# Optimization experiments

Measured on AMD Instinct MI355X. Metric: run time of the kernel, lower is better.

## Reference

```python
import jax, jax.numpy as jnp
import numpy as np

B, T, D, H, E = 2, 1024, 1024, 4096, 8


def setup_inputs() -> dict:
    key = jax.random.key(0)
    ks = jax.random.split(key, 6)
    x = jax.random.normal(ks[0], (B, T, D), dtype=jnp.float32)
    padding_mask = jnp.zeros((B, T), dtype=bool)
    # Gate: Linear(D, E, bias=False) -> weight (E, D)
    Wg = jax.random.normal(ks[1], (E, D), dtype=jnp.float32) * (1.0 / np.sqrt(D))
    # Stacked expert FFN params (torch Linear layout: weight (out, in))
    W1 = jax.random.normal(ks[2], (E, H, D), dtype=jnp.float32) * (1.0 / np.sqrt(D))
    b1 = jax.random.normal(ks[3], (E, H), dtype=jnp.float32) * 0.01
    W2 = jax.random.normal(ks[4], (E, D, H), dtype=jnp.float32) * (1.0 / np.sqrt(H))
    b2 = jax.random.normal(ks[5], (E, D), dtype=jnp.float32) * 0.01
    return {"x": x, "padding_mask": padding_mask, "Wg": Wg, "W1": W1, "b1": b1, "W2": W2, "b2": b2}


def _top2_gate(xt, pm, Wg):
    # xt: (nt, D) flattened tokens, pm: (nt,) bool padding mask
    nt, ec = xt.shape[0], Wg.shape[0]
    logits = (xt @ Wg.T).astype(jnp.float32)            # use_fp32=True
    gate_value = jax.nn.softmax(logits, axis=-1)        # (nt, E)
    gate_value = jnp.where(pm[:, None], 0.0, gate_value)
    top2_idx = jax.lax.top_k(gate_value, 2)[1]          # (nt, 2)
    keep = jax.nn.one_hot(top2_idx, ec, dtype=bool).any(axis=1)  # (nt, E) True at top1/top2
    gate_weights = jnp.where(keep, gate_value, 0.0)
    s = gate_weights.sum(axis=1, keepdims=True)
    s = jnp.where(s == 0.0, 1.0, s)
    gate_weights = gate_weights / s
    # load-balance loss: fraction of top-1 assignments vs mean gate prob per expert
    nt_real = (~pm).sum().astype(jnp.float32)
    top1_counts = (jax.nn.one_hot(top2_idx[:, 0], ec, dtype=jnp.float32)
                   * (~pm)[:, None].astype(jnp.float32)).sum(axis=0)  # (E,)
    lb_loss = ec * ((top1_counts / nt_real) * (gate_value.sum(axis=0) / nt_real)).sum()
    return lb_loss, gate_weights, gate_value


def reference(x, padding_mask, Wg, W1, b1, W2, b2):
    Bx, Tx, Dx = x.shape
    xt = x.reshape(-1, Dx)                   # (nt, D)
    pm = padding_mask.reshape(-1)            # (nt,)
    lb_loss, gw, gate_value = _top2_gate(xt, pm, Wg)
    gw = gw.astype(x.dtype)                  # (nt, E)
    # Expert FFNs (dense over experts; routing weights are zero except top-2)
    h = jax.nn.relu(jnp.einsum('nd,ehd->neh', xt, W1) + b1)   # (nt, E, H)
    y = jnp.einsum('neh,edh->ned', h, W2) + b2                # (nt, E, D)
    out = jnp.einsum('ne,ned->nd', gw, y).reshape(Bx, Tx, Dx)
    return out, gate_value, lb_loss
```

## Files before the change

kernel.cpp:

```cpp
#include <hip/hip_runtime.h>
#include <hip/hip_bf16.h>
#include <stdint.h>


#define NTOK 2048
#define DDIM 1024
#define HDIM 4096
#define NEXP 8
#define KSPLIT 2

typedef float  f32x4  __attribute__((ext_vector_type(4)));
typedef __bf16 bf16x8 __attribute__((ext_vector_type(8)));
typedef __bf16 bf16x4 __attribute__((ext_vector_type(4)));

typedef const __attribute__((address_space(1))) void g1_t;
typedef __attribute__((address_space(3))) void l3_t;
__device__ __forceinline__ void gld16(const void* g, void* l) {
  __builtin_amdgcn_global_load_lds((g1_t*)g, (l3_t*)l, 16, 0, 0);
}

__global__ void init_kernel(int* fill) {
  int t = threadIdx.x;
  if (t < NEXP) fill[t] = 0;
}

__global__ __launch_bounds__(256)
void zero_y_kernel(float* __restrict__ y) {
  size_t i = (size_t)blockIdx.x * 256 + threadIdx.x;
  ((f32x4*)y)[i] = (f32x4){0.f, 0.f, 0.f, 0.f};
}

__global__ __launch_bounds__(256)
void gate_kernel(const float* __restrict__ x, const unsigned char* __restrict__ pmask,
                 const float* __restrict__ Wg, float* __restrict__ gate_out,
                 int* __restrict__ tix, float* __restrict__ twt,
                 __bf16* __restrict__ xbf)
{
  int wave = threadIdx.x >> 6, lane = threadIdx.x & 63;
  int t = blockIdx.x * 4 + wave;
  const f32x4* x4 = (const f32x4*)(x + (size_t)t * DDIM);
  const f32x4* w4 = (const f32x4*)Wg;
  bf16x4* xb4 = (bf16x4*)(xbf + (size_t)t * DDIM);
  float acc[NEXP];
#pragma unroll
  for (int e = 0; e < NEXP; ++e) acc[e] = 0.f;
#pragma unroll
  for (int i = 0; i < 4; ++i) {
    f32x4 xv = x4[i * 64 + lane];
    bf16x4 xo;
#pragma unroll
    for (int q = 0; q < 4; ++q) xo[q] = (__bf16)xv[q];
    xb4[i * 64 + lane] = xo;
#pragma unroll
    for (int e = 0; e < NEXP; ++e) {
      f32x4 wv = w4[e * 256 + i * 64 + lane];
      acc[e] += xv[0]*wv[0] + xv[1]*wv[1] + xv[2]*wv[2] + xv[3]*wv[3];
    }
  }
#pragma unroll
  for (int e = 0; e < NEXP; ++e) {
    float v = acc[e];
#pragma unroll
    for (int off = 32; off > 0; off >>= 1) v += __shfl_xor(v, off, 64);
    acc[e] = v;
  }
  if (lane == 0) {
    bool pm = pmask[t] != 0;
    float m = acc[0];
#pragma unroll
    for (int e = 1; e < NEXP; ++e) m = fmaxf(m, acc[e]);
    float g[NEXP]; float s = 0.f;
#pragma unroll
    for (int e = 0; e < NEXP; ++e) { g[e] = expf(acc[e] - m); s += g[e]; }
    float inv = 1.f / s;
#pragma unroll
    for (int e = 0; e < NEXP; ++e) g[e] *= inv;
    if (pm) {
#pragma unroll
      for (int e = 0; e < NEXP; ++e) g[e] = 0.f;
    }
    int i1 = 0;
#pragma unroll
    for (int e = 1; e < NEXP; ++e) if (g[e] > g[i1]) i1 = e;
    int i2 = -1;
#pragma unroll
    for (int e = 0; e < NEXP; ++e) if (e != i1 && (i2 < 0 || g[e] > g[i2])) i2 = e;
    float w1 = g[i1], w2 = g[i2], ss = w1 + w2;
    if (ss == 0.f) ss = 1.f;
    w1 /= ss; w2 /= ss;
#pragma unroll
    for (int e = 0; e < NEXP; ++e) gate_out[(size_t)t * NEXP + e] = g[e];
    tix[2*t] = i1; tix[2*t+1] = i2;
    twt[2*t] = w1; twt[2*t+1] = w2;
  }
}

__global__ __launch_bounds__(1024)
void stats_kernel(const float* __restrict__ gate_out, const int* __restrict__ tix,
                  const unsigned char* __restrict__ pmask,
                  int* __restrict__ ecount, int* __restrict__ offs,
                  float* __restrict__ lb_out)
{
  int tid = threadIdx.x, lane = tid & 63, wv = tid >> 6;
  float lg[NEXP]; float lt1[NEXP]; int lec[NEXP]; float ln = 0.f;
#pragma unroll
  for (int e = 0; e < NEXP; ++e) { lg[e] = 0.f; lt1[e] = 0.f; lec[e] = 0; }
#pragma unroll
  for (int it = 0; it < NTOK / 1024; ++it) {
    int t = tid + it * 1024;
    f32x4 g0 = ((const f32x4*)(gate_out + (size_t)t * NEXP))[0];
    f32x4 g1 = ((const f32x4*)(gate_out + (size_t)t * NEXP))[1];
    lg[0] += g0[0]; lg[1] += g0[1]; lg[2] += g0[2]; lg[3] += g0[3];
    lg[4] += g1[0]; lg[5] += g1[1]; lg[6] += g1[2]; lg[7] += g1[3];
    if (!pmask[t]) {
      int i1 = tix[2*t], i2 = tix[2*t+1];
      lt1[i1] += 1.f; lec[i1] += 1; lec[i2] += 1; ln += 1.f;
    }
  }
#pragma unroll
  for (int e = 0; e < NEXP; ++e) {
#pragma unroll
    for (int off = 32; off > 0; off >>= 1) {
      lg[e]  += __shfl_xor(lg[e],  off, 64);
      lt1[e] += __shfl_xor(lt1[e], off, 64);
      lec[e] += __shfl_xor(lec[e], off, 64);
    }
  }
#pragma unroll
  for (int off = 32; off > 0; off >>= 1) ln += __shfl_xor(ln, off, 64);
  __shared__ float sg[16][NEXP], st[16][NEXP], sn[16];
  __shared__ int   se[16][NEXP];
  if (lane == 0) {
#pragma unroll
    for (int e = 0; e < NEXP; ++e) { sg[wv][e] = lg[e]; st[wv][e] = lt1[e]; se[wv][e] = lec[e]; }
    sn[wv] = ln;
  }
  __syncthreads();
  if (tid == 0) {
    float G[NEXP] = {0}, T1[NEXP] = {0}; int EC[NEXP] = {0}; float N = 0.f;
    for (int w = 0; w < 16; ++w) {
      N += sn[w];
#pragma unroll
      for (int e = 0; e < NEXP; ++e) { G[e] += sg[w][e]; T1[e] += st[w][e]; EC[e] += se[w][e]; }
    }
    int o = 0;
    for (int e = 0; e < NEXP; ++e) { ecount[e] = EC[e]; offs[e] = o; o += EC[e]; }
    if (N <= 0.f) N = 1.f;
    float lb = 0.f;
    for (int e = 0; e < NEXP; ++e) lb += (T1[e] / N) * (G[e] / N);
    lb_out[0] = (float)NEXP * lb;
  }
}

__global__ __launch_bounds__(256)
void compact_kernel(const unsigned char* __restrict__ pmask, const int* __restrict__ tix,
                    const int* __restrict__ offs, int* __restrict__ fill,
                    int* __restrict__ tok_list, int* __restrict__ slot_of)
{
  int t = blockIdx.x * 256 + threadIdx.x;
  int lane = threadIdx.x & 63;
  bool pm = pmask[t] != 0;
#pragma unroll
  for (int j = 0; j < 2; ++j) {
    int e = pm ? -1 : tix[2*t + j];
    int pos = -1;
#pragma unroll
    for (int ex = 0; ex < NEXP; ++ex) {
      unsigned long long mask = __ballot(e == ex);
      if (mask) {
        int leader = (int)(__ffsll((long long)mask) - 1);
        int base = 0;
        if (lane == leader) base = atomicAdd(&fill[ex], (int)__popcll(mask));
        base = __shfl(base, leader, 64);
        if (e == ex)
          pos = offs[ex] + base + (int)__popcll(mask & ((1ull << lane) - 1ull));
      }
    }
    if (e >= 0) { tok_list[pos] = t; slot_of[2*t + j] = pos; }
    else slot_of[2*t + j] = -1;
  }
}


#define B_STAGE_LOAD(breg, bp, koff)                                   \
  _Pragma("unroll")                                                    \
  for (int q = 0; q < 4; ++q) breg[q] = *(const f32x4*)(bp[q] + (koff));

#define B_STAGE_WRITE(dstBs, breg)                                     \
  _Pragma("unroll")                                                    \
  for (int q = 0; q < 4; ++q) {                                        \
    bf16x4 o;                                                          \
    o[0] = (__bf16)breg[q][0]; o[1] = (__bf16)breg[q][1];              \
    o[2] = (__bf16)breg[q][2]; o[3] = (__bf16)breg[q][3];              \
    *(bf16x4*)&(dstBs)[bwofs[q]] = o;                                  \
  }

__global__ __launch_bounds__(256)
void gemm1_kernel(const __bf16* __restrict__ xbf, const float* __restrict__ W1,
                  const float* __restrict__ b1, const int* __restrict__ ecount,
                  const int* __restrict__ offs, const int* __restrict__ tok_list,
                  __bf16* __restrict__ hbuf)
{
  const int NTILE = HDIM / 128;
  const int MTILE = NTOK / 128;
  int bid = blockIdx.x;
  int e = bid / (MTILE * NTILE);
  int rem = bid % (MTILE * NTILE);
  int mt = rem / NTILE, nt = rem % NTILE;
  int cnt = ecount[e];
  if (mt * 128 >= cnt) return;
  int off = offs[e];

  __shared__ __bf16 As[2][128 * 32];
  __shared__ __bf16 Bs[2][128 * 32];

  int tid = threadIdx.x, lane = tid & 63, wave = tid >> 6;
  int wm = wave >> 1, wn = wave & 1;

  const __bf16* aP[2];
#pragma unroll
  for (int c = 0; c < 2; ++c) {
    int row = c * 64 + (tid >> 2);
    int cd = (tid & 3) ^ ((row >> 1) & 3);
    int mrow = mt * 128 + row;
    int tok = tok_list[off + ((mrow < cnt) ? mrow : 0)];
    aP[c] = xbf + (size_t)tok * DDIM + cd * 8;
  }
  const float* bp[4];
  int bwofs[4];
#pragma unroll
  for (int q = 0; q < 4; ++q) {
    int r = (tid >> 3) + 32 * q;
    bp[q] = W1 + (size_t)e * HDIM * DDIM + (size_t)(nt * 128 + r) * DDIM + (tid & 7) * 4;
    int cd = (tid & 7) >> 1, h = tid & 1;
    bwofs[q] = r * 32 + ((cd ^ ((r >> 1) & 3)) << 3) + h * 4;
  }
  int cg = ((lane >> 4) ^ ((lane >> 1) & 3)) << 3;

  f32x4 acc[4][4];
#pragma unroll
  for (int m = 0; m < 4; ++m)
#pragma unroll
    for (int n = 0; n < 4; ++n) acc[m][n] = (f32x4){0.f, 0.f, 0.f, 0.f};

  const int NIT = DDIM / 32;
  f32x4 breg[4];
#pragma unroll
  for (int c = 0; c < 2; ++c) gld16(aP[c], &As[0][(c * 64 + wave * 16) * 32]);
  B_STAGE_LOAD(breg, bp, 0)
  B_STAGE_WRITE(Bs[0], breg)
  __syncthreads();

  for (int it = 0; it < NIT; ++it) {
    int cur = it & 1, nxt = cur ^ 1;
    if (it + 1 < NIT) {
      int k0 = (it + 1) * 32;
#pragma unroll
      for (int c = 0; c < 2; ++c) gld16(aP[c] + k0, &As[nxt][(c * 64 + wave * 16) * 32]);
      B_STAGE_LOAD(breg, bp, k0)
    }
    bf16x8 af[4], bfr[4];
#pragma unroll
    for (int m = 0; m < 4; ++m) af[m]  = *(const bf16x8*)&As[cur][(wm*64 + m*16 + (lane & 15)) * 32 + cg];
#pragma unroll
    for (int n = 0; n < 4; ++n) bfr[n] = *(const bf16x8*)&Bs[cur][(wn*64 + n*16 + (lane & 15)) * 32 + cg];
#pragma unroll
    for (int m = 0; m < 4; ++m)
#pragma unroll
      for (int n = 0; n < 4; ++n)
        acc[m][n] = __builtin_amdgcn_mfma_f32_16x16x32_bf16(af[m], bfr[n], acc[m][n], 0, 0, 0);
    if (it + 1 < NIT) { B_STAGE_WRITE(Bs[nxt], breg) }
    __syncthreads();
  }

#pragma unroll
  for (int n = 0; n < 4; ++n) {
    int col = nt * 128 + wn * 64 + n * 16 + (lane & 15);
    float bias = b1[e * HDIM + col];
#pragma unroll
    for (int m = 0; m < 4; ++m) {
#pragma unroll
      for (int j = 0; j < 4; ++j) {
        int mr = mt * 128 + wm * 64 + m * 16 + ((lane >> 4) << 2) + j;
        if (mr < cnt) {
          float v = fmaxf(acc[m][n][j] + bias, 0.f);
          hbuf[(size_t)(off + mr) * HDIM + col] = (__bf16)v;
        }
      }
    }
  }
}

__global__ __launch_bounds__(256)
void gemm2_kernel(const __bf16* __restrict__ hbuf, const float* __restrict__ W2,
                  const int* __restrict__ ecount, const int* __restrict__ offs,
                  float* __restrict__ ybuf)
{
  const int NTILE = DDIM / 128;
  const int MTILE = NTOK / 128;
  int bid = blockIdx.x;
  int e = bid / (MTILE * NTILE * KSPLIT);
  int rem = bid % (MTILE * NTILE * KSPLIT);
  int mt = rem / (NTILE * KSPLIT);
  int rem2 = rem % (NTILE * KSPLIT);
  int nt = rem2 / KSPLIT, kc = rem2 % KSPLIT;
  int cnt = ecount[e];
  if (mt * 128 >= cnt) return;
  int off = offs[e];

  __shared__ __bf16 As[2][128 * 32];
  __shared__ __bf16 Bs[2][128 * 32];

  int tid = threadIdx.x, lane = tid & 63, wave = tid >> 6;
  int wm = wave >> 1, wn = wave & 1;

  const __bf16* aP[2];
#pragma unroll
  for (int c = 0; c < 2; ++c) {
    int row = c * 64 + (tid >> 2);
    int cd = (tid & 3) ^ ((row >> 1) & 3);
    aP[c] = hbuf + (size_t)(off + mt * 128 + row) * HDIM + cd * 8;
  }
  const float* bp[4];
  int bwofs[4];
#pragma unroll
  for (int q = 0; q < 4; ++q) {
    int r = (tid >> 3) + 32 * q;
    bp[q] = W2 + (size_t)e * DDIM * HDIM + (size_t)(nt * 128 + r) * HDIM + (tid & 7) * 4;
    int cd = (tid & 7) >> 1, h = tid & 1;
    bwofs[q] = r * 32 + ((cd ^ ((r >> 1) & 3)) << 3) + h * 4;
  }
  int cg = ((lane >> 4) ^ ((lane >> 1) & 3)) << 3;

  f32x4 acc[4][4];
#pragma unroll
  for (int m = 0; m < 4; ++m)
#pragma unroll
    for (int n = 0; n < 4; ++n) acc[m][n] = (f32x4){0.f, 0.f, 0.f, 0.f};

  const int KCH = HDIM / KSPLIT;
  const int NIT = KCH / 32;
  int kbeg = kc * KCH;
  f32x4 breg[4];
#pragma unroll
  for (int c = 0; c < 2; ++c) gld16(aP[c] + kbeg, &As[0][(c * 64 + wave * 16) * 32]);
  B_STAGE_LOAD(breg, bp, kbeg)
  B_STAGE_WRITE(Bs[0], breg)
  __syncthreads();

  for (int it = 0; it < NIT; ++it) {
    int cur = it & 1, nxt = cur ^ 1;
    if (it + 1 < NIT) {
      int k0 = kbeg + (it + 1) * 32;
#pragma unroll
      for (int c = 0; c < 2; ++c) gld16(aP[c] + k0, &As[nxt][(c * 64 + wave * 16) * 32]);
      B_STAGE_LOAD(breg, bp, k0)
    }
    bf16x8 af[4], bfr[4];
#pragma unroll
    for (int m = 0; m < 4; ++m) af[m]  = *(const bf16x8*)&As[cur][(wm*64 + m*16 + (lane & 15)) * 32 + cg];
#pragma unroll
    for (int n = 0; n < 4; ++n) bfr[n] = *(const bf16x8*)&Bs[cur][(wn*64 + n*16 + (lane & 15)) * 32 + cg];
#pragma unroll
    for (int m = 0; m < 4; ++m)
#pragma unroll
      for (int n = 0; n < 4; ++n)
        acc[m][n] = __builtin_amdgcn_mfma_f32_16x16x32_bf16(af[m], bfr[n], acc[m][n], 0, 0, 0);
    if (it + 1 < NIT) { B_STAGE_WRITE(Bs[nxt], breg) }
    __syncthreads();
  }

#pragma unroll
  for (int m = 0; m < 4; ++m) {
#pragma unroll
    for (int j = 0; j < 4; ++j) {
      int mr = mt * 128 + wm * 64 + m * 16 + ((lane >> 4) << 2) + j;
      if (mr >= cnt) continue;
      int slot = off + mr;
#pragma unroll
      for (int n = 0; n < 4; ++n) {
        int col = nt * 128 + wn * 64 + n * 16 + (lane & 15);
        atomicAdd(&ybuf[(size_t)slot * DDIM + col], acc[m][n][j]);
      }
    }
  }
}

__global__ __launch_bounds__(256)
void combine_kernel(const float* __restrict__ ybuf, const int* __restrict__ slot_of,
                    const int* __restrict__ tix, const float* __restrict__ twt,
                    const float* __restrict__ b2, float* __restrict__ out)
{
  int t = blockIdx.x;
  int d4 = threadIdx.x;
  int sA = slot_of[2*t], sB = slot_of[2*t + 1];
  f32x4 r = (f32x4){0.f, 0.f, 0.f, 0.f};
  if (sA >= 0) {
    float wA = twt[2*t];
    f32x4 y = ((const f32x4*)(ybuf + (size_t)sA * DDIM))[d4];
    f32x4 b = ((const f32x4*)(b2 + (size_t)tix[2*t] * DDIM))[d4];
    r += wA * (y + b);
  }
  if (sB >= 0) {
    float wB = twt[2*t + 1];
    f32x4 y = ((const f32x4*)(ybuf + (size_t)sB * DDIM))[d4];
    f32x4 b = ((const f32x4*)(b2 + (size_t)tix[2*t + 1] * DDIM))[d4];
    r += wB * (y + b);
  }
  ((f32x4*)(out + (size_t)t * DDIM))[d4] = r;
}

extern "C" void kernel_launch(void* const* d_in, const int* in_sizes, int n_in,
                              void* d_out, int out_size, void* d_ws, size_t ws_size,
                              hipStream_t stream)
{
  const float* x  = (const float*)d_in[0];
  const unsigned char* pm = (const unsigned char*)d_in[1];
  const float* Wg = (const float*)d_in[2];
  const float* W1 = (const float*)d_in[3];
  const float* b1 = (const float*)d_in[4];
  const float* W2 = (const float*)d_in[5];
  const float* b2 = (const float*)d_in[6];
  float* out = (float*)d_out;
  float* gate_out = out + (size_t)NTOK * DDIM;
  float* lb_out = gate_out + (size_t)NTOK * NEXP;

  char* w = (char*)d_ws;
  int*   ecount   = (int*)(w + 0);
  int*   offs     = (int*)(w + 64);
  int*   fill     = (int*)(w + 128);
  int*   tix      = (int*)(w + 512);
  float* twt      = (float*)(w + 512 + 16384);
  int*   tok_list = (int*)(w + 512 + 32768);
  int*   slot_of  = (int*)(w + 512 + 49152);
  uintptr_t p = ((uintptr_t)(w + 512 + 65536) + 255) & ~(uintptr_t)255;
  __bf16* xbf  = (__bf16*)p;
  p += (size_t)NTOK * DDIM * 2;
  __bf16* hbuf = (__bf16*)p;
  p += (size_t)(2 * NTOK + 128) * HDIM * 2;
  float*  ybuf = (float*)p;

  init_kernel<<<1, 64, 0, stream>>>(fill);
  zero_y_kernel<<<(2 * NTOK * DDIM / 4) / 256, 256, 0, stream>>>(ybuf);
  gate_kernel<<<NTOK / 4, 256, 0, stream>>>(x, pm, Wg, gate_out, tix, twt, xbf);
  stats_kernel<<<1, 1024, 0, stream>>>(gate_out, tix, pm, ecount, offs, lb_out);
  compact_kernel<<<NTOK / 256, 256, 0, stream>>>(pm, tix, offs, fill, tok_list, slot_of);
  gemm1_kernel<<<NEXP * (NTOK / 128) * (HDIM / 128), 256, 0, stream>>>(xbf, W1, b1, ecount, offs, tok_list, hbuf);
  gemm2_kernel<<<NEXP * (NTOK / 128) * (DDIM / 128) * KSPLIT, 256, 0, stream>>>(hbuf, W2, ecount, offs, ybuf);
  combine_kernel<<<NTOK, 256, 0, stream>>>(ybuf, slot_of, tix, twt, b2, out);
}
```

Measured before the change: 293.5 us.

## Triple-buffer LDS with two-ahead prefetch and manual waitcnt in expert GEMMs

Replaces the double-buffered K loop in both expert GEMM kernels with a three-stage LDS ring. Each iteration prefetches two tiles ahead, using ping-pong fp32 register stages for B and direct-to-LDS loads for A. Raw s_barrier and explicit vmcnt/lgkmcnt waits replace __syncthreads, so global loads stay in flight across iterations and more memory latency is hidden behind MFMA work. In exchange, LDS use rises by half and register pressure grows from the second B register stage. Correctness now depends on the hand-counted waitcnt values.

```diff
diff --git a/kernel.cpp b/kernel.cpp
--- a/kernel.cpp
+++ b/kernel.cpp
@@ -182,17 +182,53 @@
 }
 
 
-#define B_STAGE_LOAD(breg, bp, koff)                                   \
+#define B_LOAD(REG, koff)                                              \
   _Pragma("unroll")                                                    \
-  for (int q = 0; q < 4; ++q) breg[q] = *(const f32x4*)(bp[q] + (koff));
-
-#define B_STAGE_WRITE(dstBs, breg)                                     \
+  for (int q = 0; q < 4; ++q) REG[q] = *(const f32x4*)(bp[q] + (koff));
+
+#define B_WRITE(dst, REG)                                              \
   _Pragma("unroll")                                                    \
   for (int q = 0; q < 4; ++q) {                                        \
     bf16x4 o;                                                          \
-    o[0] = (__bf16)breg[q][0]; o[1] = (__bf16)breg[q][1];              \
-    o[2] = (__bf16)breg[q][2]; o[3] = (__bf16)breg[q][3];              \
-    *(bf16x4*)&(dstBs)[bwofs[q]] = o;                                  \
+    o[0] = (__bf16)REG[q][0]; o[1] = (__bf16)REG[q][1];                \
+    o[2] = (__bf16)REG[q][2]; o[3] = (__bf16)REG[q][3];                \
+    *(bf16x4*)&(dst)[bwofs[q]] = o;                                    \
+  }
+
+#define FRAG_MFMA(cur)                                                               \
+  {                                                                                  \
+    bf16x8 af[4], bfr[4];                                                            \
+    _Pragma("unroll")                                                                \
+    for (int m = 0; m < 4; ++m)                                                      \
+      af[m]  = *(const bf16x8*)&As[cur][(wm*64 + m*16 + (lane & 15)) * 32 + cg];     \
+    _Pragma("unroll")                                                                \
+    for (int n = 0; n < 4; ++n)                                                      \
+      bfr[n] = *(const bf16x8*)&Bs[cur][(wn*64 + n*16 + (lane & 15)) * 32 + cg];     \
+    _Pragma("unroll")                                                                \
+    for (int m = 0; m < 4; ++m)                                                      \
+      _Pragma("unroll")                                                              \
+      for (int n = 0; n < 4; ++n)                                                    \
+        acc[m][n] = __builtin_amdgcn_mfma_f32_16x16x32_bf16(af[m], bfr[n], acc[m][n], 0, 0, 0); \
+  }
+
+#define GITER(t, NITc, WREG, LREG)                                     \
+  {                                                                    \
+    if ((t) == (NITc) - 1) asm volatile("s_waitcnt vmcnt(0)" ::: "memory"); \
+    else                   asm volatile("s_waitcnt vmcnt(6)" ::: "memory"); \
+    __builtin_amdgcn_s_barrier();                                      \
+    __builtin_amdgcn_sched_barrier(0);                                 \
+    if ((t) + 2 < (NITc)) {                                            \
+      int k2 = kb0 + ((t) + 2) * 32;                                   \
+      B_LOAD(LREG, k2)                                                 \
+      int nb = ((t) + 2) % 3;                                          \
+      gld16(aP[0] + k2, &As[nb][wave * 512]);                          \
+      gld16(aP[1] + k2, &As[nb][2048 + wave * 512]);                   \
+    }                                                                  \
+    FRAG_MFMA((t) % 3)                                                 \
+    if ((t) + 1 < (NITc)) {                                            \
+      B_WRITE(Bs[((t) + 1) % 3], WREG)                                 \
+      asm volatile("s_waitcnt lgkmcnt(0)" ::: "memory");               \
+    }                                                                  \
   }
 
 __global__ __launch_bounds__(256)
@@ -211,8 +247,8 @@
   if (mt * 128 >= cnt) return;
   int off = offs[e];
 
-  __shared__ __bf16 As[2][128 * 32];
-  __shared__ __bf16 Bs[2][128 * 32];
+  __shared__ __bf16 As[3][128 * 32];
+  __shared__ __bf16 Bs[3][128 * 32];
 
   int tid = threadIdx.x, lane = tid & 63, wave = tid >> 6;
   int wm = wave >> 1, wn = wave & 1;
@@ -244,33 +280,20 @@
     for (int n = 0; n < 4; ++n) acc[m][n] = (f32x4){0.f, 0.f, 0.f, 0.f};
 
   const int NIT = DDIM / 32;
-  f32x4 breg[4];
-#pragma unroll
-  for (int c = 0; c < 2; ++c) gld16(aP[c], &As[0][(c * 64 + wave * 16) * 32]);
-  B_STAGE_LOAD(breg, bp, 0)
-  B_STAGE_WRITE(Bs[0], breg)
-  __syncthreads();
-
-  for (int it = 0; it < NIT; ++it) {
-    int cur = it & 1, nxt = cur ^ 1;
-    if (it + 1 < NIT) {
-      int k0 = (it + 1) * 32;
-#pragma unroll
-      for (int c = 0; c < 2; ++c) gld16(aP[c] + k0, &As[nxt][(c * 64 + wave * 16) * 32]);
-      B_STAGE_LOAD(breg, bp, k0)
-    }
-    bf16x8 af[4], bfr[4];
-#pragma unroll
-    for (int m = 0; m < 4; ++m) af[m]  = *(const bf16x8*)&As[cur][(wm*64 + m*16 + (lane & 15)) * 32 + cg];
-#pragma unroll
-    for (int n = 0; n < 4; ++n) bfr[n] = *(const bf16x8*)&Bs[cur][(wn*64 + n*16 + (lane & 15)) * 32 + cg];
-#pragma unroll
-    for (int m = 0; m < 4; ++m)
-#pragma unroll
-      for (int n = 0; n < 4; ++n)
-        acc[m][n] = __builtin_amdgcn_mfma_f32_16x16x32_bf16(af[m], bfr[n], acc[m][n], 0, 0, 0);
-    if (it + 1 < NIT) { B_STAGE_WRITE(Bs[nxt], breg) }
-    __syncthreads();
+  const int kb0 = 0;
+  f32x4 bregA[4], bregB[4];
+  B_LOAD(bregA, 0)
+  gld16(aP[0], &As[0][wave * 512]);
+  gld16(aP[1], &As[0][2048 + wave * 512]);
+  B_LOAD(bregB, 32)
+  gld16(aP[0] + 32, &As[1][wave * 512]);
+  gld16(aP[1] + 32, &As[1][2048 + wave * 512]);
+  B_WRITE(Bs[0], bregA)
+  asm volatile("s_waitcnt lgkmcnt(0)" ::: "memory");
+
+  for (int tt = 0; tt < NIT; tt += 2) {
+    GITER(tt,     NIT, bregB, bregA)
+    GITER(tt + 1, NIT, bregA, bregB)
   }
 
 #pragma unroll
@@ -308,8 +331,8 @@
   if (mt * 128 >= cnt) return;
   int off = offs[e];
 
-  __shared__ __bf16 As[2][128 * 32];
-  __shared__ __bf16 Bs[2][128 * 32];
+  __shared__ __bf16 As[3][128 * 32];
+  __shared__ __bf16 Bs[3][128 * 32];
 
   int tid = threadIdx.x, lane = tid & 63, wave = tid >> 6;
   int wm = wave >> 1, wn = wave & 1;
@@ -338,36 +361,21 @@
 #pragma unroll
     for (int n = 0; n < 4; ++n) acc[m][n] = (f32x4){0.f, 0.f, 0.f, 0.f};
 
-  const int KCH = HDIM / KSPLIT;
-  const int NIT = KCH / 32;
-  int kbeg = kc * KCH;
-  f32x4 breg[4];
-#pragma unroll
-  for (int c = 0; c < 2; ++c) gld16(aP[c] + kbeg, &As[0][(c * 64 + wave * 16) * 32]);
-  B_STAGE_LOAD(breg, bp, kbeg)
-  B_STAGE_WRITE(Bs[0], breg)
-  __syncthreads();
-
-  for (int it = 0; it < NIT; ++it) {
-    int cur = it & 1, nxt = cur ^ 1;
-    if (it + 1 < NIT) {
-      int k0 = kbeg + (it + 1) * 32;
-#pragma unroll
-      for (int c = 0; c < 2; ++c) gld16(aP[c] + k0, &As[nxt][(c * 64 + wave * 16) * 32]);
-      B_STAGE_LOAD(breg, bp, k0)
-    }
-    bf16x8 af[4], bfr[4];
-#pragma unroll
-    for (int m = 0; m < 4; ++m) af[m]  = *(const bf16x8*)&As[cur][(wm*64 + m*16 + (lane & 15)) * 32 + cg];
-#pragma unroll
-    for (int n = 0; n < 4; ++n) bfr[n] = *(const bf16x8*)&Bs[cur][(wn*64 + n*16 + (lane & 15)) * 32 + cg];
-#pragma unroll
-    for (int m = 0; m < 4; ++m)
-#pragma unroll
-      for (int n = 0; n < 4; ++n)
-        acc[m][n] = __builtin_amdgcn_mfma_f32_16x16x32_bf16(af[m], bfr[n], acc[m][n], 0, 0, 0);
-    if (it + 1 < NIT) { B_STAGE_WRITE(Bs[nxt], breg) }
-    __syncthreads();
+  const int NIT = (HDIM / KSPLIT) / 32;
+  const int kb0 = kc * (HDIM / KSPLIT);
+  f32x4 bregA[4], bregB[4];
+  B_LOAD(bregA, kb0)
+  gld16(aP[0] + kb0, &As[0][wave * 512]);
+  gld16(aP[1] + kb0, &As[0][2048 + wave * 512]);
+  B_LOAD(bregB, kb0 + 32)
+  gld16(aP[0] + kb0 + 32, &As[1][wave * 512]);
+  gld16(aP[1] + kb0 + 32, &As[1][2048 + wave * 512]);
+  B_WRITE(Bs[0], bregA)
+  asm volatile("s_waitcnt lgkmcnt(0)" ::: "memory");
+
+  for (int tt = 0; tt < NIT; tt += 2) {
+    GITER(tt,     NIT, bregB, bregA)
+    GITER(tt + 1, NIT, bregA, bregB)
   }
 
 #pragma unroll
```

New measurement: 349.2 us. 19.0% more time.
